# Optimization experiments

Hardware: AMD Instinct MI355X
Metric: run time of the kernel (lower is better)

## Reference

```python
import jax, jax.numpy as jnp
import numpy as np

B, T, W, HP = 1, 64, 88, 48   # batch, frames, pitches, hidden_per_pitch
NU, NH, K = 24, 4, 25          # n_unit, n_heads, neighborhood window
HD = NU // NH                  # head dim = 6
HL = NU // 2                   # LSTM hidden per direction = 12


def _lstm_bidir(x, w_ih, w_hh, b_ih, b_hh):
    # x: [N, T, In]; w_ih: [2, 4*HL, In]; w_hh: [2, 4*HL, HL]; biases: [2, 4*HL]
    N = x.shape[0]
    def run(Wih, Whh, bih, bhh, reverse):
        def step(carry, xt):
            h, c = carry
            g = xt @ Wih.T + h @ Whh.T + bih + bhh
            i, f, gg, o = jnp.split(g, 4, axis=-1)  # torch gate order i,f,g,o
            c = jax.nn.sigmoid(f) * c + jax.nn.sigmoid(i) * jnp.tanh(gg)
            h = jax.nn.sigmoid(o) * jnp.tanh(c)
            return (h, c), h
        init = (jnp.zeros((N, HL), x.dtype), jnp.zeros((N, HL), x.dtype))
        _, ys = jax.lax.scan(step, init, jnp.swapaxes(x, 0, 1), reverse=reverse)
        return jnp.swapaxes(ys, 0, 1)
    return jnp.concatenate([run(w_ih[0], w_hh[0], b_ih[0], b_hh[0], False),
                            run(w_ih[1], w_hh[1], b_ih[1], b_hh[1], True)], axis=-1)


def _natten2d(x, qkv_w, qkv_b, rpb, proj_w, proj_b):
    # Neighborhood attention over 2D grid [B, Hh, Ww] with KxK window clamped at borders.
    Bn, Hh, Ww, C = x.shape
    qkv = (x @ qkv_w.T + qkv_b).reshape(Bn, Hh, Ww, 3, NH, HD)
    q = qkv[..., 0, :, :] * (HD ** -0.5)
    k = qkv[..., 1, :, :]
    v = qkv[..., 2, :, :]
    half = K // 2
    ar = jnp.arange(K)
    idx_i = jnp.clip(jnp.arange(Hh) - half, 0, Hh - K)[:, None] + ar  # [Hh,K]
    idx_j = jnp.clip(jnp.arange(Ww) - half, 0, Ww - K)[:, None] + ar  # [Ww,K]
    kg = k[:, idx_i][:, :, :, idx_j]  # [B,Hh,K,Ww,K,NH,HD]
    vg = v[:, idx_i][:, :, :, idx_j]
    ri = idx_i - jnp.arange(Hh)[:, None] + (K - 1)  # relative pos bias indices [Hh,K]
    rj = idx_j - jnp.arange(Ww)[:, None] + (K - 1)  # [Ww,K]
    bias = rpb[:, ri][:, :, :, rj]                  # [NH,Hh,K,Ww,K]
    logits = jnp.einsum('bijnd,biajcnd->bnijac', q, kg)
    logits = logits + jnp.transpose(bias, (0, 1, 3, 2, 4))[None]
    attn = jax.nn.softmax(logits.reshape(Bn, NH, Hh, Ww, K * K), axis=-1)
    attn = attn.reshape(Bn, NH, Hh, Ww, K, K)
    out = jnp.einsum('bnijac,biajcnd->bijnd', attn, vg).reshape(Bn, Hh, Ww, C)
    return out @ proj_w.T + proj_b


def _forward(features, condition, mask, emb, w_ih_l0, w_hh_l0, b_ih_l0, b_hh_l0,
             w_ih_l1, w_hh_l1, b_ih_l1, b_hh_l1, qkv_w, qkv_b, rpb, proj_w, proj_b,
             out_w, out_b):
    # concat: [B,T,88,HP] + [B,T,88,4] + [B,T,88,1] -> [B,T,88,HP+5]
    cat = jnp.concatenate([jnp.transpose(features, (0, 1, 3, 2)), emb[condition],
                           mask[..., None]], axis=-1)
    x = jnp.transpose(cat, (0, 2, 1, 3)).reshape(B * W, T, HP + 5)  # pitchwise LSTM
    x = _lstm_bidir(x, w_ih_l0, w_hh_l0, b_ih_l0, b_hh_l0)
    x = _lstm_bidir(x, w_ih_l1, w_hh_l1, b_ih_l1, b_hh_l1)
    x = jnp.transpose(x.reshape(B, W, T, NU), (0, 2, 1, 3))  # [B,T,88,NU]
    for _ in range(2):  # n_layers=2; Sequential(*[m]*2) => SHARED weights
        x = _natten2d(x, qkv_w, qkv_b, rpb, proj_w, proj_b)
    return x @ out_w.T + out_b  # [B,T,88,5]


def setup_inputs():
    ks = jax.random.split(jax.random.key(0), 24)
    def unif(k, shape, fan):
        s = 1.0 / np.sqrt(fan)
        return jax.random.uniform(k, shape, jnp.float32, -s, s)
    return {
        'features': jax.random.normal(ks[0], (B, T, HP, W), jnp.float32),
        'condition': jax.random.randint(ks[1], (B, T, W), 0, 5),
        'mask': jax.random.uniform(ks[2], (B, T, W), jnp.float32),
        'emb': jax.random.normal(ks[3], (5, 4), jnp.float32),
        'w_ih_l0': unif(ks[4], (2, 4 * HL, HP + 5), HL),
        'w_hh_l0': unif(ks[5], (2, 4 * HL, HL), HL),
        'b_ih_l0': unif(ks[6], (2, 4 * HL), HL),
        'b_hh_l0': unif(ks[7], (2, 4 * HL), HL),
        'w_ih_l1': unif(ks[8], (2, 4 * HL, 2 * HL), HL),
        'w_hh_l1': unif(ks[9], (2, 4 * HL, HL), HL),
        'b_ih_l1': unif(ks[10], (2, 4 * HL), HL),
        'b_hh_l1': unif(ks[11], (2, 4 * HL), HL),
        'qkv_w': unif(ks[12], (3 * NU, NU), NU),
        'qkv_b': unif(ks[13], (3 * NU,), NU),
        'rpb': jax.random.normal(ks[14], (NH, 2 * K - 1, 2 * K - 1), jnp.float32) * 0.02,
        'proj_w': unif(ks[15], (NU, NU), NU),
        'proj_b': unif(ks[16], (NU,), NU),
        'out_w': unif(ks[17], (5, NU), NU),
        'out_b': unif(ks[18], (5,), NU),
    }


def reference(features, condition, mask, emb, w_ih_l0, w_hh_l0, b_ih_l0, b_hh_l0,
              w_ih_l1, w_hh_l1, b_ih_l1, b_hh_l1, qkv_w, qkv_b, rpb, proj_w, proj_b,
              out_w, out_b):
    return _forward(features, condition, mask, emb, w_ih_l0, w_hh_l0, b_ih_l0, b_hh_l0,
                    w_ih_l1, w_hh_l1, b_ih_l1, b_hh_l1, qkv_w, qkv_b, rpb,
                    proj_w, proj_b, out_w, out_b)
```

## Files before the change

kernel.cpp:

```cpp
#include <hip/hip_runtime.h>
#include <hip/hip_bf16.h>

#define NPIX (64*88)
#define NSEQ 88
#define TT 64
#define F0 53
#define GATES 48

typedef __hip_bfloat16 bf16;

__device__ __forceinline__ float frcp(float x){ return __builtin_amdgcn_rcpf(x); }
__device__ __forceinline__ float blo(unsigned u){ return __uint_as_float(u<<16); }
__device__ __forceinline__ float bhi(unsigned u){ return __uint_as_float(u & 0xffff0000u); }

__device__ __forceinline__ float rl(float v, int l){
  return __int_as_float(__builtin_amdgcn_readlane(__float_as_int(v), l));
}
template<int K> __device__ __forceinline__ float qbcast(float v){
  constexpr int ctrl = K | (K<<2) | (K<<4) | (K<<6);
  return __int_as_float(__builtin_amdgcn_update_dpp(0, __float_as_int(v), ctrl, 0xf, 0xf, true));
}

template<int CTRL> __device__ __forceinline__ float dpp_add(float v){
  return v + __int_as_float(__builtin_amdgcn_update_dpp(0, __float_as_int(v), CTRL, 0xf, 0xf, true));
}
template<int CTRL> __device__ __forceinline__ float dpp_max(float v){
  int vi = __float_as_int(v);
  return fmaxf(v, __int_as_float(__builtin_amdgcn_update_dpp(vi, vi, CTRL, 0xf, 0xf, false)));
}
__device__ __forceinline__ float wred_sum(float v){
  v = dpp_add<0x111>(v); v = dpp_add<0x112>(v); v = dpp_add<0x114>(v); v = dpp_add<0x118>(v);
  v = dpp_add<0x142>(v); v = dpp_add<0x143>(v);
  return rl(v,63);
}
__device__ __forceinline__ float wred_max(float v){
  v = dpp_max<0x111>(v); v = dpp_max<0x112>(v); v = dpp_max<0x114>(v); v = dpp_max<0x118>(v);
  v = dpp_max<0x142>(v); v = dpp_max<0x143>(v);
  return rl(v,63);
}

__device__ __forceinline__ void lstm_dir(const float* __restrict__ whh,
    const float* gb_base, float* ybuf, int d, int lane){
  int u = lane >> 2, grp = lane & 3;
  int uc = (u < 12) ? u : 11;
  int j = grp*12 + uc;
  float w[12];
  const float* wb = whh + (d*GATES + j)*12;
  #pragma unroll
  for (int m=0;m<12;++m) w[m] = wb[m];
  float negs = (grp==2) ? -2.f : -1.f;
  float amul = (grp==2) ?  2.f :  1.f;
  float aadd = (grp==2) ? -1.f :  0.f;
  const float* gb = gb_base + (d*TT)*49 + j;
  float hval = 0.f, cval = 0.f;
  int t0 = d ? (TT-1) : 0;
  float gnext = gb[t0*49];
  bool wr = (grp==0) && (u < 12);
  for (int s=0;s<TT;++s){
    int t = d ? (TT-1-s) : s;
    float gg = gnext;
    int tn = d ? max(TT-2-s,0) : min(s+1,TT-1);
    gnext = gb[tn*49];
    float h0=rl(hval,0),  h1=rl(hval,4),  h2=rl(hval,8),   h3=rl(hval,12);
    float h4=rl(hval,16), h5=rl(hval,20), h6=rl(hval,24),  h7=rl(hval,28);
    float h8=rl(hval,32), h9=rl(hval,36), h10=rl(hval,40), h11=rl(hval,44);
    float a0 = gg + h0*w[0] + h4*w[4] + h8*w[8];
    float a1 = h1*w[1] + h5*w[5] + h9*w[9];
    float a2 = h2*w[2] + h6*w[6] + h10*w[10];
    float a3 = h3*w[3] + h7*w[7] + h11*w[11];
    float dot = (a0+a1)+(a2+a3);
    float act = amul*frcp(1.f + __expf(negs*dot)) + aadd;
    float ai = qbcast<0>(act);
    float af = qbcast<1>(act);
    float ag = qbcast<2>(act);
    float ao = qbcast<3>(act);
    float cn = af*cval + ai*ag;
    float th = 2.f*frcp(1.f + __expf(-2.f*cn)) - 1.f;
    hval = ao*th; cval = cn;
    if (wr) ybuf[t*25 + d*12 + u] = hval;
  }
}

__global__ __launch_bounds__(1024) void k_core(
    const float* __restrict__ feat, const int* __restrict__ cond,
    const float* __restrict__ mask, const float* __restrict__ emb,
    const float* __restrict__ wih0, const float* __restrict__ whh0,
    const float* __restrict__ bih0, const float* __restrict__ bhh0,
    const float* __restrict__ wih1, const float* __restrict__ whh1,
    const float* __restrict__ bih1, const float* __restrict__ bhh1,
    const float* __restrict__ qkv_w, const float* __restrict__ qkv_b,
    float* __restrict__ q, bf16* __restrict__ kh, bf16* __restrict__ vh){
  int n = (blockIdx.x & 7)*11 + (blockIdx.x >> 3);
  int tid = threadIdx.x;
  int wave = tid >> 6; int lane = tid & 63;
  __shared__ float smem[12864];
  float* gbuf = smem;
  float* sx   = smem + 6272;
  float* y0   = smem + 6272+3392;
  float* y1   = smem + 6272+4992;
  float* outb = smem;

  for (int idx = tid; idx < TT*F0; idx += 1024){
    int t = idx / F0, f = idx - t*F0;
    float v;
    if (f < 48)      v = feat[(t*48 + f)*88 + n];
    else if (f < 52) v = emb[cond[t*88+n]*4 + (f-48)];
    else             v = mask[t*88+n];
    sx[idx] = v;
  }
  __syncthreads();

  {
    int wu = __builtin_amdgcn_readfirstlane(wave);
    int dd = wu >> 3, jg = wu & 7;
    const float* w0 = wih0 + (dd*GATES + jg*6)*F0;
    const float* xr = sx + lane*F0;
    float a0[6], a1[6];
    #pragma unroll
    for (int k=0;k<6;++k){
      int j = dd*GATES + jg*6 + k;
      a0[k] = bih0[j] + bhh0[j];
      a1[k] = 0.f;
    }
    for (int f=0; f<52; f+=2){
      float x0 = xr[f], x1 = xr[f+1];
      #pragma unroll
      for (int k=0;k<6;++k){
        a0[k] += x0*w0[k*F0+f];
        a1[k] += x1*w0[k*F0+f+1];
      }
    }
    {
      float x0 = xr[52];
      #pragma unroll
      for (int k=0;k<6;++k) a0[k] += x0*w0[k*F0+52];
    }
    float* go = gbuf + (dd*TT + lane)*49 + jg*6;
    #pragma unroll
    for (int k=0;k<6;++k) go[k] = a0[k] + a1[k];
  }
  __syncthreads();

  if (wave < 2) lstm_dir(whh0, gbuf, y0, wave, lane);
  __syncthreads();

  {
    int wu = __builtin_amdgcn_readfirstlane(wave);
    int dd = wu >> 3, jg = wu & 7;
    const float* w1p = wih1 + (dd*GATES + jg*6)*24;
    const float* xr = y0 + lane*25;
    float a0[6], a1[6];
    #pragma unroll
    for (int k=0;k<6;++k){
      int j = dd*GATES + jg*6 + k;
      a0[k] = bih1[j] + bhh1[j];
      a1[k] = 0.f;
    }
    #pragma unroll
    for (int c=0; c<24; c+=2){
      float x0 = xr[c], x1 = xr[c+1];
      #pragma unroll
      for (int k=0;k<6;++k){
        a0[k] += x0*w1p[k*24+c];
        a1[k] += x1*w1p[k*24+c+1];
      }
    }
    float* go = gbuf + (dd*TT + lane)*49 + jg*6;
    #pragma unroll
    for (int k=0;k<6;++k) go[k] = a0[k] + a1[k];
  }
  __syncthreads();

  if (wave < 2) lstm_dir(whh1, gbuf, y1, wave, lane);
  __syncthreads();

  if (wave < 12){
    int wu = __builtin_amdgcn_readfirstlane(wave);
    int g0 = wu*6;
    const float* qw = qkv_w + g0*24;
    const float* xr = y1 + lane*25;
    float a0[6], a1[6];
    #pragma unroll
    for (int k=0;k<6;++k){ a0[k] = qkv_b[g0+k]; a1[k] = 0.f; }
    #pragma unroll
    for (int c=0; c<24; c+=2){
      float x0 = xr[c], x1 = xr[c+1];
      #pragma unroll
      for (int k=0;k<6;++k){
        a0[k] += x0*qw[k*24+c];
        a1[k] += x1*qw[k*24+c+1];
      }
    }
    float* oo = outb + lane*73 + g0;
    #pragma unroll
    for (int k=0;k<6;++k) oo[k] = a0[k] + a1[k];
  }
  __syncthreads();

  for (int idx = tid; idx < TT*72; idx += 1024){
    int gq = idx % 72; int t = idx / 72;
    int p = t*88 + n;
    float acc = outb[t*73 + gq];
    int s = gq/24, rem = gq - s*24;
    if (s==0) q[p*24+rem] = acc*0.4082482904638631f;
    else {
      int hh = rem/6, pos = rem - hh*6;
      bf16* dst = (s==1) ? kh : vh;
      dst[((size_t)hh*NPIX + p)*8 + pos] = __float2bfloat16(acc);
    }
  }
}

template<int MODE>
__global__ __launch_bounds__(1024, 8) void k_natten(
    const float* __restrict__ q, const bf16* __restrict__ kh,
    const bf16* __restrict__ vh, const float* __restrict__ rpb,
    const float* __restrict__ pw, const float* __restrict__ pb,
    const float* __restrict__ qkv_w, const float* __restrict__ qkv_b,
    const float* __restrict__ ow, const float* __restrict__ ob,
    float* __restrict__ q2, bf16* __restrict__ kh2, bf16* __restrict__ vh2,
    float* __restrict__ out){
  int bid = blockIdx.x;
  int b = (bid & 7)*176 + (bid >> 3);
  int ti = b / 44, tj = b - ti*44;
  int i0 = ti*2, j0 = tj*2;
  int tid = threadIdx.x;
  int w = tid >> 6; int lane = tid & 63;
  int osi = min(max(i0-12,0),39);
  int osj = min(max(j0-12,0),63);

  __shared__ unsigned kv[16224];
  unsigned* kt = kv;
  unsigned* vt = kv + 8112;
  float* aop = (float*)kv;
  float* x4  = aop + 96;

  const uint4* kg = (const uint4*)kh;
  const uint4* vg = (const uint4*)vh;
  for (int idx = tid; idx < 2704; idx += 1024){
    int h = idx / 676; int r = idx - h*676;
    int a = r / 26, cc = r - a*26;
    int gi = min(osi + a, 63), gj = min(osj + cc, 87);
    int src = h*NPIX + gi*88 + gj;
    uint4 kr = kg[src];
    uint4 vr = vg[src];
    int o = idx*3;
    kt[o] = kr.x; kt[o+1] = kr.y; kt[o+2] = kr.z;
    vt[o] = vr.x; vt[o+1] = vr.y; vt[o+2] = vr.z;
  }
  __syncthreads();

  int px = w & 3; int h = w >> 2;
  int pi = i0 + (px>>1), pj = j0 + (px&1);
  int p = pi*88 + pj;
  int dsi = min(max(pi-12,0),39) - osi;
  int dsj = min(max(pj-12,0),63) - osj;
  int rbi = osi + dsi - pi + 24;
  int rbj = osj + dsj - pj + 24;
  int hbase = h*2028;
  int rowofs = hbase + (dsi*26 + dsj)*3;
  const float* rpbh = rpb + (h*49 + rbi)*49 + rbj;

  float qv[6];
  #pragma unroll
  for (int d=0; d<6; ++d) qv[d] = q[p*24 + h*6 + d];

  float lgv[10];
  float lmax = -1e30f;
  #pragma unroll
  for (int it=0; it<10; ++it){
    int nb = lane + it*64;
    bool valid = nb < 625;
    int nbc = valid ? nb : 624;
    int a = nbc/25, cc = nbc - a*25;
    int r3 = rowofs + (a*26 + cc)*3;
    unsigned k0 = kt[r3], k1 = kt[r3+1], k2 = kt[r3+2];
    float lg = qv[0]*blo(k0)+qv[1]*bhi(k0)+qv[2]*blo(k1)
             + qv[3]*bhi(k1)+qv[4]*blo(k2)+qv[5]*bhi(k2);
    lg += rpbh[a*49 + cc];
    lg = valid ? lg : -1e30f;
    lgv[it] = lg;
    lmax = fmaxf(lmax, lg);
  }
  lmax = wred_max(lmax);
  float lsum = 0.f;
  #pragma unroll
  for (int it=0; it<10; ++it){
    float pe = __expf(lgv[it]-lmax);
    lgv[it] = pe; lsum += pe;
  }
  lsum = wred_sum(lsum);
  float acc[6] = {0,0,0,0,0,0};
  #pragma unroll
  for (int it=0; it<10; ++it){
    int nb = lane + it*64;
    int nbc = (nb < 625) ? nb : 624;
    int a = nbc/25, cc = nbc - a*25;
    int r3 = rowofs + (a*26 + cc)*3;
    unsigned v0 = vt[r3], v1 = vt[r3+1], v2 = vt[r3+2];
    float pe = lgv[it];
    acc[0] += pe*blo(v0); acc[1] += pe*bhi(v0);
    acc[2] += pe*blo(v1); acc[3] += pe*bhi(v1);
    acc[4] += pe*blo(v2); acc[5] += pe*bhi(v2);
  }
  float inv = frcp(lsum);
  #pragma unroll
  for (int d=0; d<6; ++d) acc[d] = wred_sum(acc[d])*inv;

  __syncthreads();
  if (lane == 0){
    #pragma unroll
    for (int d=0; d<6; ++d) aop[px*24 + h*6 + d] = acc[d];
  }
  __syncthreads();

  if (tid < 96){
    int pp = tid / 24, c = tid - (tid/24)*24;
    float a2 = pb[c];
    const float* wr = pw + c*24;
    #pragma unroll
    for (int k=0;k<24;++k) a2 += aop[pp*24+k]*wr[k];
    x4[pp*24+c] = a2;
  }
  __syncthreads();

  if (MODE == 0){
    if (tid < 288){
      int pp = tid / 72, g = tid - (tid/72)*72;
      float a2 = qkv_b[g];
      const float* wr = qkv_w + g*24;
      #pragma unroll
      for (int k=0;k<24;++k) a2 += x4[pp*24+k]*wr[k];
      int ppi = i0 + (pp>>1), ppj = j0 + (pp&1);
      int pp_ = ppi*88 + ppj;
      int s = g/24, rem = g - s*24;
      if (s==0) q2[pp_*24+rem] = a2*0.4082482904638631f;
      else {
        int hh = rem/6, pos = rem - hh*6;
        bf16* dst = (s==1) ? kh2 : vh2;
        dst[((size_t)hh*NPIX + pp_)*8 + pos] = __float2bfloat16(a2);
      }
    }
  } else {
    if (tid < 20){
      int pp = tid / 5, c = tid - (tid/5)*5;
      float a2 = ob[c];
      const float* wr = ow + c*24;
      #pragma unroll
      for (int k=0;k<24;++k) a2 += x4[pp*24+k]*wr[k];
      int ppi = i0 + (pp>>1), ppj = j0 + (pp&1);
      out[(ppi*88 + ppj)*5 + c] = a2;
    }
  }
}

extern "C" void kernel_launch(void* const* d_in, const int* in_sizes, int n_in,
                              void* d_out, int out_size, void* d_ws, size_t ws_size,
                              hipStream_t stream) {
  const float* feat    = (const float*)d_in[0];
  const int*   cond    = (const int*)  d_in[1];
  const float* mask    = (const float*)d_in[2];
  const float* emb     = (const float*)d_in[3];
  const float* w_ih_l0 = (const float*)d_in[4];
  const float* w_hh_l0 = (const float*)d_in[5];
  const float* b_ih_l0 = (const float*)d_in[6];
  const float* b_hh_l0 = (const float*)d_in[7];
  const float* w_ih_l1 = (const float*)d_in[8];
  const float* w_hh_l1 = (const float*)d_in[9];
  const float* b_ih_l1 = (const float*)d_in[10];
  const float* b_hh_l1 = (const float*)d_in[11];
  const float* qkv_w   = (const float*)d_in[12];
  const float* qkv_b   = (const float*)d_in[13];
  const float* rpb     = (const float*)d_in[14];
  const float* proj_w  = (const float*)d_in[15];
  const float* proj_b  = (const float*)d_in[16];
  const float* out_w   = (const float*)d_in[17];
  const float* out_b   = (const float*)d_in[18];
  float* out = (float*)d_out;

  float* ws  = (float*)d_ws;
  float* Q1  = ws;
  float* Q2  = Q1 + 135168;
  bf16*  KH1 = (bf16*)(Q2 + 135168);
  bf16*  VH1 = KH1 + 180224;
  bf16*  KH2 = VH1 + 180224;
  bf16*  VH2 = KH2 + 180224;

  k_core<<<NSEQ, 1024, 0, stream>>>(
      feat, cond, mask, emb,
      w_ih_l0, w_hh_l0, b_ih_l0, b_hh_l0,
      w_ih_l1, w_hh_l1, b_ih_l1, b_hh_l1,
      qkv_w, qkv_b, Q1, KH1, VH1);

  k_natten<0><<<32*44, 1024, 0, stream>>>(
      Q1, KH1, VH1, rpb, proj_w, proj_b, qkv_w, qkv_b,
      nullptr, nullptr, Q2, KH2, VH2, nullptr);

  k_natten<1><<<32*44, 1024, 0, stream>>>(
      Q2, KH2, VH2, rpb, proj_w, proj_b, nullptr, nullptr,
      out_w, out_b, nullptr, nullptr, nullptr, out);
}
```

Before: 178.5 us.

## Halve natten block size with two tasks per wave and row-pair lane mapping

The neighborhood-attention kernel now runs 512 threads per block, and each wave handles two (pixel, head) tasks in sequence. Lanes are mapped so that 50 of them cover two 25-wide window rows per iteration (13 iterations), which replaces the per-element divide-by-25 with fixed strides. The LSTM cell pre-scales its weights and gate inputs by log2(e) so it can call exp2 directly. Launch bounds and an unroll pragma are also adjusted. This trades per-block parallelism for less index math and fewer idle lanes, but 14 of 64 lanes now sit idle on every iteration.

```diff
diff --git a/kernel.cpp b/kernel.cpp
--- a/kernel.cpp
+++ b/kernel.cpp
@@ -6,10 +6,12 @@
 #define TT 64
 #define F0 53
 #define GATES 48
+#define LOG2E 1.4426950408889634f
 
 typedef __hip_bfloat16 bf16;
 
 __device__ __forceinline__ float frcp(float x){ return __builtin_amdgcn_rcpf(x); }
+__device__ __forceinline__ float fexp2(float x){ return __builtin_amdgcn_exp2f(x); }
 __device__ __forceinline__ float blo(unsigned u){ return __uint_as_float(u<<16); }
 __device__ __forceinline__ float bhi(unsigned u){ return __uint_as_float(u & 0xffff0000u); }
 
@@ -47,7 +49,7 @@
   float w[12];
   const float* wb = whh + (d*GATES + j)*12;
   #pragma unroll
-  for (int m=0;m<12;++m) w[m] = wb[m];
+  for (int m=0;m<12;++m) w[m] = wb[m]*LOG2E;
   float negs = (grp==2) ? -2.f : -1.f;
   float amul = (grp==2) ?  2.f :  1.f;
   float aadd = (grp==2) ? -1.f :  0.f;
@@ -69,19 +71,19 @@
     float a2 = h2*w[2] + h6*w[6] + h10*w[10];
     float a3 = h3*w[3] + h7*w[7] + h11*w[11];
     float dot = (a0+a1)+(a2+a3);
-    float act = amul*frcp(1.f + __expf(negs*dot)) + aadd;
+    float act = amul*frcp(1.f + fexp2(negs*dot)) + aadd;
     float ai = qbcast<0>(act);
     float af = qbcast<1>(act);
     float ag = qbcast<2>(act);
     float ao = qbcast<3>(act);
     float cn = af*cval + ai*ag;
-    float th = 2.f*frcp(1.f + __expf(-2.f*cn)) - 1.f;
+    float th = 2.f*frcp(1.f + fexp2(-2.885390081777927f*cn)) - 1.f;
     hval = ao*th; cval = cn;
     if (wr) ybuf[t*25 + d*12 + u] = hval;
   }
 }
 
-__global__ __launch_bounds__(1024) void k_core(
+__global__ __launch_bounds__(1024, 4) void k_core(
     const float* __restrict__ feat, const int* __restrict__ cond,
     const float* __restrict__ mask, const float* __restrict__ emb,
     const float* __restrict__ wih0, const float* __restrict__ whh0,
@@ -122,6 +124,7 @@
       a0[k] = bih0[j] + bhh0[j];
       a1[k] = 0.f;
     }
+    #pragma unroll
     for (int f=0; f<52; f+=2){
       float x0 = xr[f], x1 = xr[f+1];
       #pragma unroll
@@ -137,7 +140,7 @@
     }
     float* go = gbuf + (dd*TT + lane)*49 + jg*6;
     #pragma unroll
-    for (int k=0;k<6;++k) go[k] = a0[k] + a1[k];
+    for (int k=0;k<6;++k) go[k] = (a0[k] + a1[k])*LOG2E;
   }
   __syncthreads();
 
@@ -167,7 +170,7 @@
     }
     float* go = gbuf + (dd*TT + lane)*49 + jg*6;
     #pragma unroll
-    for (int k=0;k<6;++k) go[k] = a0[k] + a1[k];
+    for (int k=0;k<6;++k) go[k] = (a0[k] + a1[k])*LOG2E;
   }
   __syncthreads();
 
@@ -212,7 +215,7 @@
 }
 
 template<int MODE>
-__global__ __launch_bounds__(1024, 8) void k_natten(
+__global__ __launch_bounds__(512, 4) void k_natten(
     const float* __restrict__ q, const bf16* __restrict__ kh,
     const bf16* __restrict__ vh, const float* __restrict__ rpb,
     const float* __restrict__ pw, const float* __restrict__ pb,
@@ -237,7 +240,7 @@
 
   const uint4* kg = (const uint4*)kh;
   const uint4* vg = (const uint4*)vh;
-  for (int idx = tid; idx < 2704; idx += 1024){
+  for (int idx = tid; idx < 2704; idx += 512){
     int h = idx / 676; int r = idx - h*676;
     int a = r / 26, cc = r - a*26;
     int gi = min(osi + a, 63), gj = min(osj + cc, 87);
@@ -250,67 +253,79 @@
   }
   __syncthreads();
 
-  int px = w & 3; int h = w >> 2;
-  int pi = i0 + (px>>1), pj = j0 + (px&1);
-  int p = pi*88 + pj;
-  int dsi = min(max(pi-12,0),39) - osi;
-  int dsj = min(max(pj-12,0),63) - osj;
-  int rbi = osi + dsi - pi + 24;
-  int rbj = osj + dsj - pj + 24;
-  int hbase = h*2028;
-  int rowofs = hbase + (dsi*26 + dsj)*3;
-  const float* rpbh = rpb + (h*49 + rbi)*49 + rbj;
-
-  float qv[6];
+  int lrow = (lane >= 25 && lane < 50) ? 1 : 0;
+  int lcc  = lane - (lane >= 50 ? 50 : (lane >= 25 ? 25 : 0));
+  bool lact = lane < 50;
+
+  float oacc[2][6];
   #pragma unroll
-  for (int d=0; d<6; ++d) qv[d] = q[p*24 + h*6 + d];
-
-  float lgv[10];
-  float lmax = -1e30f;
-  #pragma unroll
-  for (int it=0; it<10; ++it){
-    int nb = lane + it*64;
-    bool valid = nb < 625;
-    int nbc = valid ? nb : 624;
-    int a = nbc/25, cc = nbc - a*25;
-    int r3 = rowofs + (a*26 + cc)*3;
-    unsigned k0 = kt[r3], k1 = kt[r3+1], k2 = kt[r3+2];
-    float lg = qv[0]*blo(k0)+qv[1]*bhi(k0)+qv[2]*blo(k1)
-             + qv[3]*bhi(k1)+qv[4]*blo(k2)+qv[5]*bhi(k2);
-    lg += rpbh[a*49 + cc];
-    lg = valid ? lg : -1e30f;
-    lgv[it] = lg;
-    lmax = fmaxf(lmax, lg);
-  }
-  lmax = wred_max(lmax);
-  float lsum = 0.f;
-  #pragma unroll
-  for (int it=0; it<10; ++it){
-    float pe = __expf(lgv[it]-lmax);
-    lgv[it] = pe; lsum += pe;
-  }
-  lsum = wred_sum(lsum);
-  float acc[6] = {0,0,0,0,0,0};
-  #pragma unroll
-  for (int it=0; it<10; ++it){
-    int nb = lane + it*64;
-    int nbc = (nb < 625) ? nb : 624;
-    int a = nbc/25, cc = nbc - a*25;
-    int r3 = rowofs + (a*26 + cc)*3;
-    unsigned v0 = vt[r3], v1 = vt[r3+1], v2 = vt[r3+2];
-    float pe = lgv[it];
-    acc[0] += pe*blo(v0); acc[1] += pe*bhi(v0);
-    acc[2] += pe*blo(v1); acc[3] += pe*bhi(v1);
-    acc[4] += pe*blo(v2); acc[5] += pe*bhi(v2);
-  }
-  float inv = frcp(lsum);
-  #pragma unroll
-  for (int d=0; d<6; ++d) acc[d] = wred_sum(acc[d])*inv;
+  for (int task=0; task<2; ++task){
+    int tw = w + task*8;
+    int px = tw & 3; int h = tw >> 2;
+    int pi = i0 + (px>>1), pj = j0 + (px&1);
+    int p = pi*88 + pj;
+    int dsi = min(max(pi-12,0),39) - osi;
+    int dsj = min(max(pj-12,0),63) - osj;
+    int rbi = osi + dsi - pi + 24;
+    int rbj = osj + dsj - pj + 24;
+    const float* rpbh = rpb + (h*49 + rbi)*49 + rbj;
+    int rowofs = h*2028 + (dsi*26 + dsj)*3;
+    int lds0 = rowofs + (lrow*26 + lcc)*3;
+    int rpo0 = lrow*49 + lcc;
+
+    float qv[6];
+    #pragma unroll
+    for (int d=0; d<6; ++d) qv[d] = q[p*24 + h*6 + d];
+
+    float lgv[13];
+    float lmax = -1e30f;
+    #pragma unroll
+    for (int it=0; it<13; ++it){
+      bool valid = lact && (it < 12 || lrow == 0);
+      int r3 = lds0 + it*156;
+      if (it == 12) r3 = lrow ? lds0 : r3;
+      unsigned k0 = kt[r3], k1 = kt[r3+1], k2 = kt[r3+2];
+      float lg = qv[0]*blo(k0)+qv[1]*bhi(k0)+qv[2]*blo(k1)
+               + qv[3]*bhi(k1)+qv[4]*blo(k2)+qv[5]*bhi(k2);
+      int ro = valid ? (rpo0 + it*98) : 0;
+      lg += rpbh[ro];
+      lg = valid ? lg : -1e30f;
+      lgv[it] = lg;
+      lmax = fmaxf(lmax, lg);
+    }
+    lmax = wred_max(lmax);
+    float lsum = 0.f;
+    #pragma unroll
+    for (int it=0; it<13; ++it){
+      float pe = __expf(lgv[it]-lmax);
+      lgv[it] = pe; lsum += pe;
+    }
+    lsum = wred_sum(lsum);
+    float acc[6] = {0,0,0,0,0,0};
+    #pragma unroll
+    for (int it=0; it<13; ++it){
+      int r3 = lds0 + it*156;
+      if (it == 12) r3 = lrow ? lds0 : r3;
+      unsigned v0 = vt[r3], v1 = vt[r3+1], v2 = vt[r3+2];
+      float pe = lgv[it];
+      acc[0] += pe*blo(v0); acc[1] += pe*bhi(v0);
+      acc[2] += pe*blo(v1); acc[3] += pe*bhi(v1);
+      acc[4] += pe*blo(v2); acc[5] += pe*bhi(v2);
+    }
+    float inv = frcp(lsum);
+    #pragma unroll
+    for (int d=0; d<6; ++d) oacc[task][d] = wred_sum(acc[d])*inv;
+  }
 
   __syncthreads();
   if (lane == 0){
     #pragma unroll
-    for (int d=0; d<6; ++d) aop[px*24 + h*6 + d] = acc[d];
+    for (int task=0; task<2; ++task){
+      int tw = w + task*8;
+      int px = tw & 3; int h = tw >> 2;
+      #pragma unroll
+      for (int d=0; d<6; ++d) aop[px*24 + h*6 + d] = oacc[task][d];
+    }
   }
   __syncthreads();
 
@@ -392,11 +407,11 @@
       w_ih_l1, w_hh_l1, b_ih_l1, b_hh_l1,
       qkv_w, qkv_b, Q1, KH1, VH1);
 
-  k_natten<0><<<32*44, 1024, 0, stream>>>(
+  k_natten<0><<<8*176, 512, 0, stream>>>(
       Q1, KH1, VH1, rpb, proj_w, proj_b, qkv_w, qkv_b,
       nullptr, nullptr, Q2, KH2, VH2, nullptr);
 
-  k_natten<1><<<32*44, 1024, 0, stream>>>(
+  k_natten<1><<<8*176, 512, 0, stream>>>(
       Q2, KH2, VH2, rpb, proj_w, proj_b, nullptr, nullptr,
       out_w, out_b, nullptr, nullptr, nullptr, out);
 }
```

Result: slower. 184.1 us (+3.1%).
